# Optimization experiments

Measured on AMD Instinct MI355X. Metric: run time of the kernel, lower is better.

The kernel has to match this reference:

```python
import jax, jax.numpy as jnp
import numpy as np

B, R, CIN, J, O, ITERS = 512, 1152, 8, 10, 16, 3  # batch, routes, in_ch, capsules, out_ch, routing iters


def squash(s, axis):
    # v = (||s||^2 / (1 + ||s||^2)) * s / ||s||  (standard CapsNet squash)
    sq = jnp.sum(s * s, axis=axis, keepdims=True)
    return (sq / (1.0 + sq)) * s * jax.lax.rsqrt(sq + 1e-8)


def setup_inputs() -> dict:
    key = jax.random.key(0)
    k1, k2 = jax.random.split(key)
    x = jax.random.normal(k1, (B, R, CIN), dtype=jnp.float32)
    W = jax.random.normal(k2, (R, J, O, CIN), dtype=jnp.float32)  # param, batch-broadcast
    return {"x": x, "W": W}


def reference(x, W):
    # u_hat[b,r,j,:] = W[r,j] @ x[b,r]   (replaces torch stack/cat broadcasting)
    u_hat = jnp.einsum('rjoc,brc->brjo', W, x)  # [B,R,J,O]
    b_ij = jnp.zeros((x.shape[0], R, J), dtype=x.dtype)
    v = None
    for it in range(ITERS):
        c_ij = jax.nn.softmax(b_ij, axis=2)                 # softmax over capsules j
        s_j = jnp.einsum('brj,brjo->bjo', c_ij, u_hat)      # weighted sum over routes
        v = squash(s_j, axis=-1)                            # [B,J,O]
        if it < ITERS - 1:
            b_ij = b_ij + jnp.einsum('brjo,bjo->brj', u_hat, v)  # agreement
    # torch returns v_j.squeeze(1) with shape [B, J, O, 1]
    return v[..., None]
```

## Files before the change

### kernel.cpp

```cpp
#include <hip/hip_runtime.h>
#include <hip/hip_fp16.h>
#include <cstdint>
#include <cstddef>

#define NB 512
#define NR 1152
#define NC 8
#define NJ 10
#define NO 16
#define NJO 160

typedef unsigned int uint32;

union H2U { __half2 h; uint32 u; };

__device__ __forceinline__ uint32 packf16(float a0, float a1) {
    H2U p;
    p.h = __halves2half2(__float2half_rn(a0), __float2half_rn(a1));
    return p.u;
}
__device__ __forceinline__ float2 unpackf16(uint32 w) {
    H2U p; p.u = w;
    return __half22float2(p.h);
}

__global__ __launch_bounds__(256) void xpose_kernel(const float* __restrict__ x,
                                                    float* __restrict__ xT) {
    const int r0 = blockIdx.x * 16;
    const int b0 = blockIdx.y * 64;
    const int t  = threadIdx.x;
    __shared__ float tile[16][65][8];

    for (int i = t; i < 2048; i += 256) {
        int b = i >> 5, r = (i >> 1) & 15, h = i & 1;
        float4 v = *(const float4*)&x[(size_t)(b0 + b) * (NR * NC) + (size_t)(r0 + r) * NC + h * 4];
        *(float4*)&tile[r][b][h * 4] = v;
    }
    __syncthreads();
    for (int i = t; i < 2048; i += 256) {
        int r = i >> 7, b = (i >> 1) & 63, h = i & 1;
        float4 v = *(const float4*)&tile[r][b][h * 4];
        *(float4*)&xT[(size_t)(r0 + r) * (NB * NC) + (size_t)(b0 + b) * NC + h * 4] = v;
    }
}

__global__ __launch_bounds__(320) void uhat_kernel(const float* __restrict__ xT,
                                                   const float* __restrict__ W,
                                                   uint32* __restrict__ u) {
    const int r = blockIdx.x;
    const int t = threadIdx.x;

    __shared__ float Ws[NC][NJO + 4];
    __shared__ float xs[NB][NC];

    for (int i = t; i < NJO * NC; i += 320) {
        Ws[i & 7][i >> 3] = W[(size_t)r * (NJO * NC) + i];
    }
    {
        const float4* xsrc = (const float4*)(xT + (size_t)r * (NB * NC));
        float4* xdst = (float4*)&xs[0][0];
        for (int i = t; i < (NB * NC) / 4; i += 320) xdst[i] = xsrc[i];
    }
    __syncthreads();

    const int ni   = t % 80;
    const int half = t / 80;
    const int qt  = ni / 20;
    const int rem = ni % 20;
    const int j   = rem >> 1;
    const int d   = rem & 1;
    const int jo0 = 16 * j + 4 * qt + 2 * d;

    float w0[8], w1[8];
#pragma unroll
    for (int c = 0; c < 8; ++c) {
        w0[c] = Ws[c][jo0];
        w1[c] = Ws[c][jo0 + 1];
    }

    for (int b = half; b < NB; b += 4) {
        const float4* xp = (const float4*)xs[b];
        float4 xa = xp[0], xb = xp[1];
        float a0 = w0[0] * xa.x + w0[1] * xa.y + w0[2] * xa.z + w0[3] * xa.w
                 + w0[4] * xb.x + w0[5] * xb.y + w0[6] * xb.z + w0[7] * xb.w;
        float a1 = w1[0] * xa.x + w1[1] * xa.y + w1[2] * xa.z + w1[3] * xa.w
                 + w1[4] * xb.x + w1[5] * xb.y + w1[6] * xb.z + w1[7] * xb.w;
        u[(size_t)(b * NR + r) * 80 + ni] = packf16(a0, a1);
    }
}

__global__ __launch_bounds__(576, 2) void routing_kernel(const uint32* __restrict__ u,
                                                         float* __restrict__ outp) {
    const int b  = blockIdx.x;
    const int t  = threadIdx.x;
    const int w  = t >> 6;
    const int l  = t & 63;
    const int m  = (l >> 2) & 15;
    const int qt = l & 3;

    __shared__ float sl[NJO];
    __shared__ float vls[NJO];
    __shared__ float vaccl[NJO];

    for (int i = t; i < NJO; i += 576) sl[i] = 0.0f;
    __syncthreads();

    const uint32* ubase = u + (size_t)b * (NR * 80) + qt * 20;

#pragma unroll 1
    for (int it = 0; it < 3; ++it) {
        float acc[40];
#pragma unroll
        for (int i = 0; i < 40; ++i) acc[i] = 0.0f;

#pragma unroll 1
        for (int c8 = 0; c8 < 8; ++c8) {
            const int r = (w * 8 + c8) * 16 + m;
            const uint4* up = (const uint4*)(ubase + (size_t)r * 80);
            uint32 ur[20];
#pragma unroll
            for (int i = 0; i < 5; ++i) {
                uint4 q = up[i];
                ur[4 * i + 0] = q.x; ur[4 * i + 1] = q.y;
                ur[4 * i + 2] = q.z; ur[4 * i + 3] = q.w;
            }

            float cj[NJ];
            if (it == 0) {
#pragma unroll
                for (int j = 0; j < NJ; ++j) cj[j] = 0.1f;
            } else {
                float sum = 0.0f;
#pragma unroll
                for (int j = 0; j < NJ; ++j) {
                    float2 ua = unpackf16(ur[2 * j]);
                    float2 ub = unpackf16(ur[2 * j + 1]);
                    float4 vv = *(const float4*)&vls[16 * j + 4 * qt];
                    float pj = ua.x * vv.x + ua.y * vv.y + ub.x * vv.z + ub.y * vv.w;
                    pj += __shfl_xor(pj, 1);
                    pj += __shfl_xor(pj, 2);
                    float e = __expf(pj);
                    cj[j] = e;
                    sum += e;
                }
                float inv = 1.0f / sum;
#pragma unroll
                for (int j = 0; j < NJ; ++j) cj[j] *= inv;
            }

#pragma unroll
            for (int j = 0; j < NJ; ++j) {
                float2 ua = unpackf16(ur[2 * j]);
                float2 ub = unpackf16(ur[2 * j + 1]);
                acc[4 * j + 0] += cj[j] * ua.x;
                acc[4 * j + 1] += cj[j] * ua.y;
                acc[4 * j + 2] += cj[j] * ub.x;
                acc[4 * j + 3] += cj[j] * ub.y;
            }
        }

        float a[24];
        {
            const int bit = (l >> 2) & 1;
#pragma unroll
            for (int i = 0; i < 24; ++i) {
                float lo = acc[i];
                float hi = (i + 24 < 40) ? acc[i + 24] : 0.0f;
                float send = bit ? lo : hi;
                float recv = __shfl_xor(send, 4);
                a[i] = (bit ? hi : lo) + recv;
            }
        }
#pragma unroll
        for (int st = 1; st < 4; ++st) {
            const int h = 24 >> st;
            const int bit = (l >> (2 + st)) & 1;
#pragma unroll
            for (int i = 0; i < 12; ++i) {
                if (i < h) {
                    float send = bit ? a[i] : a[i + h];
                    float recv = __shfl_xor(send, 4 << st);
                    a[i] = (bit ? a[i + h] : a[i]) + recv;
                }
            }
        }
        const int base = 3 * (__brev((uint32)m) >> 28);
#pragma unroll
        for (int i = 0; i < 3; ++i) {
            int aidx = base + i;
            if (aidx < 40) {
                int j = aidx >> 2, e = aidx & 3;
                atomicAdd(&sl[16 * j + 4 * qt + e], a[i]);
            }
        }
        __syncthreads();

        if (t < 80) {
            float2 sv = *(const float2*)&sl[2 * t];
            float sq = sv.x * sv.x + sv.y * sv.y;
#pragma unroll
            for (int off = 1; off < 8; off <<= 1) sq += __shfl_xor(sq, off, 8);
            float scale = (sq / (1.0f + sq)) * rsqrtf(sq + 1e-8f);
            float vx = sv.x * scale, vy = sv.y * scale;
            if (it == 2) {
                *(float2*)&outp[b * NJO + 2 * t] = make_float2(vx, vy);
            } else {
                float2 va;
                if (it == 0) va = make_float2(vx, vy);
                else {
                    va = *(const float2*)&vaccl[2 * t];
                    va.x += vx; va.y += vy;
                }
                *(float2*)&vaccl[2 * t] = va;
                *(float2*)&vls[2 * t]   = va;
            }
        }
        __syncthreads();
        if (it < 2) {
            for (int i = t; i < NJO; i += 576) sl[i] = 0.0f;
            __syncthreads();
        }
    }
}

extern "C" void kernel_launch(void* const* d_in, const int* in_sizes, int n_in,
                              void* d_out, int out_size, void* d_ws, size_t ws_size,
                              hipStream_t stream) {
    (void)in_sizes; (void)n_in; (void)out_size; (void)ws_size;

    const float* x = (const float*)d_in[0];
    const float* W = (const float*)d_in[1];
    float* out = (float*)d_out;

    char* ws = (char*)d_ws;
    const size_t XBYTES = (size_t)NR * NB * NC * 4;
    float*  xT = (float*)ws;
    uint32* u  = (uint32*)(ws + XBYTES);

    xpose_kernel<<<dim3(NR / 16, NB / 64), 256, 0, stream>>>(x, xT);
    uhat_kernel<<<NR, 320, 0, stream>>>(xT, W, u);
    routing_kernel<<<NB, 576, 0, stream>>>(u, out);
}
```

Before: 215.2 us.

## Drop transpose kernel and vectorize u_hat stores with four outputs per thread

Removes the separate x transpose pass: uhat_kernel now gathers its route's x slice directly from the original layout with strided float4 loads. Each thread also computes four packed fp16 pairs and writes them as one 16-byte store instead of one 4-byte store. This removes one kernel launch and a full write and read of a transposed copy of x, and improves store width. In exchange the x gather becomes strided across batch rows and more weights are held in registers.

Result: slower. 259.2 us (+20.4%).

```diff
diff --git a/kernel.cpp b/kernel.cpp
--- a/kernel.cpp
+++ b/kernel.cpp
@@ -24,27 +24,7 @@
     return __half22float2(p.h);
 }
 
-__global__ __launch_bounds__(256) void xpose_kernel(const float* __restrict__ x,
-                                                    float* __restrict__ xT) {
-    const int r0 = blockIdx.x * 16;
-    const int b0 = blockIdx.y * 64;
-    const int t  = threadIdx.x;
-    __shared__ float tile[16][65][8];
-
-    for (int i = t; i < 2048; i += 256) {
-        int b = i >> 5, r = (i >> 1) & 15, h = i & 1;
-        float4 v = *(const float4*)&x[(size_t)(b0 + b) * (NR * NC) + (size_t)(r0 + r) * NC + h * 4];
-        *(float4*)&tile[r][b][h * 4] = v;
-    }
-    __syncthreads();
-    for (int i = t; i < 2048; i += 256) {
-        int r = i >> 7, b = (i >> 1) & 63, h = i & 1;
-        float4 v = *(const float4*)&tile[r][b][h * 4];
-        *(float4*)&xT[(size_t)(r0 + r) * (NB * NC) + (size_t)(b0 + b) * NC + h * 4] = v;
-    }
-}
-
-__global__ __launch_bounds__(320) void uhat_kernel(const float* __restrict__ xT,
+__global__ __launch_bounds__(320) void uhat_kernel(const float* __restrict__ x,
                                                    const float* __restrict__ W,
                                                    uint32* __restrict__ u) {
     const int r = blockIdx.x;
@@ -56,36 +36,47 @@
     for (int i = t; i < NJO * NC; i += 320) {
         Ws[i & 7][i >> 3] = W[(size_t)r * (NJO * NC) + i];
     }
-    {
-        const float4* xsrc = (const float4*)(xT + (size_t)r * (NB * NC));
-        float4* xdst = (float4*)&xs[0][0];
-        for (int i = t; i < (NB * NC) / 4; i += 320) xdst[i] = xsrc[i];
+    for (int i = t; i < 2 * NB; i += 320) {
+        int b = i >> 1, h = i & 1;
+        float4 v = *(const float4*)&x[(size_t)b * (NR * NC) + (size_t)r * NC + h * 4];
+        *(float4*)&xs[b][h * 4] = v;
     }
     __syncthreads();
 
-    const int ni   = t % 80;
-    const int half = t / 80;
-    const int qt  = ni / 20;
-    const int rem = ni % 20;
-    const int j   = rem >> 1;
-    const int d   = rem & 1;
-    const int jo0 = 16 * j + 4 * qt + 2 * d;
-
-    float w0[8], w1[8];
-#pragma unroll
-    for (int c = 0; c < 8; ++c) {
-        w0[c] = Ws[c][jo0];
-        w1[c] = Ws[c][jo0 + 1];
-    }
-
-    for (int b = half; b < NB; b += 4) {
+    const int pi   = t % 20;
+    const int half = t / 20;
+
+    float wlo[4][8], whi[4][8];
+#pragma unroll
+    for (int k = 0; k < 4; ++k) {
+        const int ni  = 4 * pi + k;
+        const int qt  = ni / 20;
+        const int rem = ni % 20;
+        const int j   = rem >> 1;
+        const int d   = rem & 1;
+        const int jo0 = 16 * j + 4 * qt + 2 * d;
+#pragma unroll
+        for (int c = 0; c < 8; ++c) {
+            wlo[k][c] = Ws[c][jo0];
+            whi[k][c] = Ws[c][jo0 + 1];
+        }
+    }
+
+#pragma unroll 2
+    for (int b = half; b < NB; b += 16) {
         const float4* xp = (const float4*)xs[b];
         float4 xa = xp[0], xb = xp[1];
-        float a0 = w0[0] * xa.x + w0[1] * xa.y + w0[2] * xa.z + w0[3] * xa.w
-                 + w0[4] * xb.x + w0[5] * xb.y + w0[6] * xb.z + w0[7] * xb.w;
-        float a1 = w1[0] * xa.x + w1[1] * xa.y + w1[2] * xa.z + w1[3] * xa.w
-                 + w1[4] * xb.x + w1[5] * xb.y + w1[6] * xb.z + w1[7] * xb.w;
-        u[(size_t)(b * NR + r) * 80 + ni] = packf16(a0, a1);
+        uint4 st;
+        uint32* stw = (uint32*)&st;
+#pragma unroll
+        for (int k = 0; k < 4; ++k) {
+            float a0 = wlo[k][0] * xa.x + wlo[k][1] * xa.y + wlo[k][2] * xa.z + wlo[k][3] * xa.w
+                     + wlo[k][4] * xb.x + wlo[k][5] * xb.y + wlo[k][6] * xb.z + wlo[k][7] * xb.w;
+            float a1 = whi[k][0] * xa.x + whi[k][1] * xa.y + whi[k][2] * xa.z + whi[k][3] * xa.w
+                     + whi[k][4] * xb.x + whi[k][5] * xb.y + whi[k][6] * xb.z + whi[k][7] * xb.w;
+            stw[k] = packf16(a0, a1);
+        }
+        *(uint4*)&u[(size_t)(b * NR + r) * 80 + 4 * pi] = st;
     }
 }
 
@@ -232,12 +223,8 @@
     const float* W = (const float*)d_in[1];
     float* out = (float*)d_out;
 
-    char* ws = (char*)d_ws;
-    const size_t XBYTES = (size_t)NR * NB * NC * 4;
-    float*  xT = (float*)ws;
-    uint32* u  = (uint32*)(ws + XBYTES);
-
-    xpose_kernel<<<dim3(NR / 16, NB / 64), 256, 0, stream>>>(x, xT);
-    uhat_kernel<<<NR, 320, 0, stream>>>(xT, W, u);
+    uint32* u = (uint32*)d_ws;
+
+    uhat_kernel<<<NR, 320, 0, stream>>>(x, W, u);
     routing_kernel<<<NB, 576, 0, stream>>>(u, out);
 }
```
